# Optimization experiments

Measured on AMD Instinct MI355X. Metric: run time of the kernel, lower is better.

The kernel has to match this reference:

```python
import jax, jax.numpy as jnp
import numpy as np

H = 16       # num query heads
KV = 4       # num kv heads
D = 64       # head_dim
EPS = 1e-6


def setup_inputs() -> dict:
    key = jax.random.key(0)
    ks = jax.random.split(key, 12)
    B, N, E = 2, 2048, 1024
    s = 0.02
    return {
        "x": jax.random.normal(ks[0], (B, N, E), jnp.float32),
        "sin": jax.random.normal(ks[1], (N, D), jnp.float32),
        "cos": jax.random.normal(ks[2], (N, D), jnp.float32),
        "wq_w": jax.random.normal(ks[3], (E, E), jnp.float32) * s,
        "wq_b": jax.random.normal(ks[4], (E,), jnp.float32) * s,
        "wk_w": jax.random.normal(ks[5], (KV * D, E), jnp.float32) * s,
        "wk_b": jax.random.normal(ks[6], (KV * D,), jnp.float32) * s,
        "wv_w": jax.random.normal(ks[7], (KV * D, E), jnp.float32) * s,
        "wv_b": jax.random.normal(ks[8], (KV * D,), jnp.float32) * s,
        "qn_w": jnp.ones((D,), jnp.float32),
        "kn_w": jnp.ones((D,), jnp.float32),
        "proj_w": jax.random.normal(ks[9], (E, E), jnp.float32) * s,
        "proj_b": jax.random.normal(ks[10], (E,), jnp.float32) * s,
    }


def _rmsnorm(t, w):
    # t: [..., D]
    var = jnp.mean(t * t, axis=-1, keepdims=True)
    return t * jax.lax.rsqrt(var + EPS) * w


def _rope(t, sin, cos):
    # t: [B,h,N,D]; sin/cos: [N,D] broadcast
    x1, x2 = jnp.split(t, 2, axis=-1)
    rotated = jnp.concatenate([-x2, x1], axis=-1)
    return t * cos + rotated * sin


def reference(x, sin, cos, wq_w, wq_b, wk_w, wk_b, wv_w, wv_b,
              qn_w, kn_w, proj_w, proj_b):
    B, N, E = x.shape
    q = (x @ wq_w.T + wq_b).reshape(B, N, H, D).transpose(0, 2, 1, 3)   # [B,H,N,D]
    k = (x @ wk_w.T + wk_b).reshape(B, N, KV, D).transpose(0, 2, 1, 3)  # [B,KV,N,D]
    v = (x @ wv_w.T + wv_b).reshape(B, N, KV, D).transpose(0, 2, 1, 3)
    q = _rmsnorm(q, qn_w)
    k = _rmsnorm(k, kn_w)
    # GQA: repeat kv heads to match query heads (repeat_interleave on head dim)
    factor = H // KV
    k = jnp.repeat(k, factor, axis=1)  # [B,H,N,D]
    v = jnp.repeat(v, factor, axis=1)
    # RoPE (n_extra = 0 since sin covers full sequence)
    q = _rope(q, sin, cos)
    k = _rope(k, sin, cos)
    # scaled dot-product attention
    scale = 1.0 / np.sqrt(D).astype(np.float32)
    scores = jnp.einsum("bhqd,bhkd->bhqk", q, k) * scale
    attn = jax.nn.softmax(scores, axis=-1)
    out = jnp.einsum("bhqk,bhkd->bhqd", attn, v)      # [B,H,N,D]
    out = out.transpose(0, 2, 1, 3).reshape(B, N, E)  # [B,N,E]
    return out @ proj_w.T + proj_b
```

## Files before the change

kernel.cpp:

```cpp
#include <hip/hip_runtime.h>
#include <hip/hip_bf16.h>
#include <math.h>


#define N_SEQ 2048
#define EMB   1024
#define NH    16
#define NKV   4
#define HD    64
#define BATCH 2
#define M_TOT 4096
#define QKV_N 1536

typedef __attribute__((ext_vector_type(8)))  short short8;
typedef __attribute__((ext_vector_type(4)))  float f32x4;
typedef __attribute__((ext_vector_type(16))) float f32x16;

__device__ __forceinline__ ushort f2bf(float f) {
    union { __hip_bfloat16 h; ushort u; } cv;
    cv.h = __float2bfloat16(f);
    return cv.u;
}
__device__ __forceinline__ float bf2f(ushort u) {
    union { __hip_bfloat16 h; ushort u; } cv;
    cv.u = u;
    return __bfloat162float(cv.h);
}
__device__ __forceinline__ uint pack2bf(float a, float b) {
    union { __hip_bfloat162 h; uint u; } cv;
    cv.h = __float22bfloat162_rn(float2{a, b});
    return cv.u;
}

__device__ __forceinline__ void cvt4(const float* __restrict__ s,
                                     ushort* __restrict__ d, long g, long gd) {
    const float4 v = ((const float4*)s)[g];
    ushort4 o;
    o.x = f2bf(v.x); o.y = f2bf(v.y); o.z = f2bf(v.z); o.w = f2bf(v.w);
    ((ushort4*)d)[gd] = o;
}

__global__ __launch_bounds__(256) void prep_kernel(
    const float* __restrict__ x,  const float* __restrict__ wq,
    const float* __restrict__ wk, const float* __restrict__ wv,
    const float* __restrict__ wp, const float* __restrict__ bq,
    const float* __restrict__ bk, const float* __restrict__ bv,
    ushort* __restrict__ xb, ushort* __restrict__ Wqkv,
    ushort* __restrict__ Wproj, float* __restrict__ bqkv)
{
    const long i = (long)blockIdx.x * 256 + threadIdx.x;
    if (i < 1048576) {
        cvt4(x, xb, i, i);
    } else if (i < 1310720) {
        const long g = i - 1048576;
        cvt4(wq, Wqkv, g, g);
    } else if (i < 1376256) {
        const long g = i - 1310720;
        cvt4(wk, Wqkv, g, 262144 + g);
    } else if (i < 1441792) {
        const long g = i - 1376256;
        cvt4(wv, Wqkv, g, 327680 + g);
    } else if (i < 1703936) {
        const long g = i - 1441792;
        cvt4(wp, Wproj, g, g);
    } else if (i < 1704320) {
        const long j = i - 1703936;
        float4 v;
        if (j < 256)      v = ((const float4*)bq)[j];
        else if (j < 320) v = ((const float4*)bk)[j - 256];
        else              v = ((const float4*)bv)[j - 320];
        ((float4*)bqkv)[j] = v;
    }
}

template <bool BF16OUT>
__global__ __launch_bounds__(256) void gemm_mfma_kernel(
    const ushort* __restrict__ A, const ushort* __restrict__ W,
    const float* __restrict__ bias, void* __restrict__ Cout,
    int K, int ldc)
{
    __shared__ ushort As[128 * 40];
    __shared__ ushort Bs[128 * 40];

    const int tid = threadIdx.x;
    const int m0 = blockIdx.y * 128, n0 = blockIdx.x * 128;
    const int w = tid >> 6, lane = tid & 63;
    const int quad = lane >> 4, l16 = lane & 15;
    const int wm = (w & 1) * 64, wn = (w >> 1) * 64;

    f32x4 acc[4][4] = {};

    float bb[4];
#pragma unroll
    for (int j = 0; j < 4; ++j) bb[j] = bias[n0 + wn + j * 16 + l16];

    const int r0 = tid >> 2;
    const int c0 = tid & 3;
    const ushort* Ap = A + (size_t)(m0 + r0) * K + c0 * 8;
    const ushort* Wp = W + (size_t)(n0 + r0) * K + c0 * 8;

    for (int k0 = 0; k0 < K; k0 += 32) {
        const short8 a0 = *(const short8*)(Ap + k0);
        const short8 a1 = *(const short8*)(Ap + (size_t)64 * K + k0);
        const short8 b0 = *(const short8*)(Wp + k0);
        const short8 b1 = *(const short8*)(Wp + (size_t)64 * K + k0);
        __syncthreads();
        *(short8*)&As[r0 * 40 + c0 * 8] = a0;
        *(short8*)&As[(r0 + 64) * 40 + c0 * 8] = a1;
        *(short8*)&Bs[r0 * 40 + c0 * 8] = b0;
        *(short8*)&Bs[(r0 + 64) * 40 + c0 * 8] = b1;
        __syncthreads();

        short8 aF[4], bF[4];
#pragma unroll
        for (int i = 0; i < 4; ++i)
            aF[i] = *(const short8*)&As[(wm + i * 16 + l16) * 40 + quad * 8];
#pragma unroll
        for (int j = 0; j < 4; ++j)
            bF[j] = *(const short8*)&Bs[(wn + j * 16 + l16) * 40 + quad * 8];
#pragma unroll
        for (int i = 0; i < 4; ++i)
#pragma unroll
            for (int j = 0; j < 4; ++j)
                acc[i][j] = __builtin_amdgcn_mfma_f32_16x16x32_bf16(
                    aF[i], bF[j], acc[i][j], 0, 0, 0);
    }

#pragma unroll
    for (int i = 0; i < 4; ++i) {
        const int rowb = m0 + wm + i * 16 + quad * 4;
#pragma unroll
        for (int j = 0; j < 4; ++j) {
            const int col = n0 + wn + j * 16 + l16;
#pragma unroll
            for (int r = 0; r < 4; ++r) {
                const float vv = acc[i][j][r] + bb[j];
                if (BF16OUT)
                    ((ushort*)Cout)[(size_t)(rowb + r) * ldc + col] = f2bf(vv);
                else
                    ((float*)Cout)[(size_t)(rowb + r) * ldc + col] = vv;
            }
        }
    }
}

__global__ __launch_bounds__(256) void norm_rope_kernel(
    const ushort* __restrict__ Tq, const float* __restrict__ qn_w,
    const float* __restrict__ kn_w, const float* __restrict__ sinp,
    const float* __restrict__ cosp, ushort* __restrict__ Qb,
    ushort* __restrict__ Kf)
{
    const int gw = (int)(((long)blockIdx.x * 256 + threadIdx.x) >> 6);
    const int lane = threadIdx.x & 63;

    const bool isQ = (gw < 65536);
    const int vec = isQ ? gw : gw - 65536;
    const int hshift = isQ ? 4 : 2;
    const int colBase = isQ ? 0 : EMB;
    const float* nw = isQ ? qn_w : kn_w;
    const float outScale = isQ ? 0.125f : 1.0f;

    const int m = vec >> hshift;
    const int h = vec & ((1 << hshift) - 1);
    const int n = m & (N_SEQ - 1);
    const int b = m >> 11;

    const float t = bf2f(Tq[(size_t)m * QKV_N + colBase + h * HD + lane]);
    float s = t * t;
#pragma unroll
    for (int mask = 32; mask; mask >>= 1) s += __shfl_xor(s, mask, 64);
    const float r = rsqrtf(s * (1.0f / 64.0f) + 1e-6f);

    const float tn = t * r * nw[lane];
    const float partner = __shfl_xor(tn, 32, 64);
    const float rot = (lane < 32) ? -partner : partner;
    const float val = (tn * cosp[n * HD + lane] + rot * sinp[n * HD + lane]) * outScale;

    if (isQ) {
        Qb[((size_t)((b << 4) + h) * N_SEQ + n) * HD + lane] = f2bf(val);
    } else {
        const int kt = n >> 6, rr = n & 63, ss = rr >> 5, l32k = rr & 31;
        const int c = lane >> 4, l5k = (lane >> 3) & 1, j = lane & 7;
        Kf[((size_t)(b * NKV + h) * 32 + kt) * 4096
           + (ss * 4 + c) * 512 + l32k * 16 + l5k * 8 + j] = f2bf(val);
    }
}

__global__ __launch_bounds__(256) void transpose_v_kernel(
    const ushort* __restrict__ Tq, ushort* __restrict__ Vf)
{
    __shared__ ushort L[64 * 72];
    const int kt = blockIdx.x;
    const int n0 = kt * 64;
    const int bkv = blockIdx.y;
    const int b = bkv >> 2, kv = bkv & 3;
    const int tid = threadIdx.x;

#pragma unroll
    for (int it = 0; it < 2; ++it) {
        const int j = tid + it * 256;
        const int r = j >> 3, c = j & 7;
        const short8 v = *(const short8*)&Tq[(size_t)(b * N_SEQ + n0 + r) * QKV_N
                                             + 1280 + kv * HD + c * 8];
        *(short8*)&L[r * 72 + c * 8] = v;
    }
    __syncthreads();
#pragma unroll
    for (int it = 0; it < 2; ++it) {
        const int j = tid + it * 256;
        const int d = j >> 3, c8 = j & 7;
        short8 o;
#pragma unroll
        for (int e = 0; e < 8; ++e) o[e] = (short)L[(c8 * 8 + e) * 72 + d];
        const int ss = c8 >> 2, tt = (c8 >> 1) & 1, l5v = c8 & 1;
        const int d2 = d >> 5, l32v = d & 31;
        *(short8*)&Vf[((size_t)bkv * 32 + kt) * 4096
                      + ((ss * 2 + tt) * 2 + d2) * 512 + l32v * 16 + l5v * 8] = o;
    }
}

__global__ __launch_bounds__(256, 4) void flash_mfma32_kernel(
    const ushort* __restrict__ Qb, const ushort* __restrict__ Kf,
    const ushort* __restrict__ Vf, ushort* __restrict__ Ob)
{
    __shared__ float fsm[4352];

    const int qt = blockIdx.x;
    const int bh = blockIdx.y;
    const int b = bh >> 4, h = bh & 15;
    const int kvh = h >> 2;
    const int tid = threadIdx.x;
    const int w = tid >> 6, lane = tid & 63;
    const int l32 = lane & 31, l5 = lane >> 5;
    const int qg = w & 1;
    const int kh = w >> 1;

    const ushort* Qg = Qb + ((size_t)bh * N_SEQ + qt * 64 + qg * 32) * HD;
    const size_t kvbase = (size_t)(b * NKV + kvh) * (32 * 4096);
    const ushort* Kp = Kf + kvbase;
    const ushort* Vp = Vf + kvbase;
    const int loff = l32 * 16 + l5 * 8;

    short8 qF[4];
#pragma unroll
    for (int c = 0; c < 4; ++c)
        qF[c] = *(const short8*)&Qg[(size_t)l32 * HD + c * 16 + l5 * 8];

    f32x16 Oa[2] = {};
    float mrow = -3.0e38f, lrow = 0.0f;

    for (int i = 0; i < 16; ++i) {
        const int kt = kh * 16 + i;
        const ushort* Kt = Kp + kt * 4096;
        const ushort* Vt = Vp + kt * 4096;

        short8 kT[2][4];
#pragma unroll
        for (int s = 0; s < 2; ++s)
#pragma unroll
            for (int c = 0; c < 4; ++c)
                kT[s][c] = *(const short8*)&Kt[(s * 4 + c) * 512 + loff];
        short8 vT[2][2][2];
#pragma unroll
        for (int s = 0; s < 2; ++s)
#pragma unroll
            for (int t = 0; t < 2; ++t)
#pragma unroll
                for (int d2 = 0; d2 < 2; ++d2)
                    vT[s][t][d2] = *(const short8*)&Vt[((s * 2 + t) * 2 + d2) * 512 + loff];

        f32x16 Sv[2] = {};
#pragma unroll
        for (int s = 0; s < 2; ++s)
#pragma unroll
            for (int c = 0; c < 4; ++c)
                Sv[s] = __builtin_amdgcn_mfma_f32_32x32x16_bf16(kT[s][c], qF[c], Sv[s], 0, 0, 0);

        float mx = -3.0e38f;
#pragma unroll
        for (int s = 0; s < 2; ++s)
#pragma unroll
            for (int r = 0; r < 16; ++r) mx = fmaxf(mx, Sv[s][r]);
        mx = fmaxf(mx, __shfl_xor(mx, 32, 64));
        const float mnew = fmaxf(mrow, mx);
        const float alpha = __expf(mrow - mnew);
        mrow = mnew;
        float rs = 0.0f;
#pragma unroll
        for (int s = 0; s < 2; ++s)
#pragma unroll
            for (int r = 0; r < 16; ++r) {
                Sv[s][r] = __expf(Sv[s][r] - mnew);
                rs += Sv[s][r];
            }
        rs += __shfl_xor(rs, 32, 64);
        lrow = lrow * alpha + rs;
#pragma unroll
        for (int t = 0; t < 2; ++t)
#pragma unroll
            for (int r = 0; r < 16; ++r) Oa[t][r] *= alpha;

        uint P2[2][8];
#pragma unroll
        for (int s = 0; s < 2; ++s)
#pragma unroll
            for (int g = 0; g < 4; ++g)
#pragma unroll
                for (int hh = 0; hh < 2; ++hh)
                    P2[s][g * 2 + hh] =
                        pack2bf(Sv[s][4 * g + 2 * hh], Sv[s][4 * g + 2 * hh + 1]);

#pragma unroll
        for (int s = 0; s < 2; ++s)
#pragma unroll
            for (int t = 0; t < 2; ++t) {
                const uint snd0 = l5 ? P2[s][4 * t + 0] : P2[s][4 * t + 2];
                const uint snd1 = l5 ? P2[s][4 * t + 1] : P2[s][4 * t + 3];
                const uint kp0  = l5 ? P2[s][4 * t + 2] : P2[s][4 * t + 0];
                const uint kp1  = l5 ? P2[s][4 * t + 3] : P2[s][4 * t + 1];
                const uint rcv0 = __shfl_xor(snd0, 32, 64);
                const uint rcv1 = __shfl_xor(snd1, 32, 64);
                union { uint u[4]; short8 s8; } pb;
                pb.u[0] = l5 ? rcv0 : kp0;
                pb.u[1] = l5 ? rcv1 : kp1;
                pb.u[2] = l5 ? kp0 : rcv0;
                pb.u[3] = l5 ? kp1 : rcv1;
#pragma unroll
                for (int d2 = 0; d2 < 2; ++d2)
                    Oa[d2] = __builtin_amdgcn_mfma_f32_32x32x16_bf16(
                        vT[s][t][d2], pb.s8, Oa[d2], 0, 0, 0);
            }
    }

    float* buf = fsm + qg * 2176;
    if (kh == 1) {
#pragma unroll
        for (int d2 = 0; d2 < 2; ++d2)
#pragma unroll
            for (int r = 0; r < 16; ++r)
                buf[(d2 * 16 + r) * 64 + lane] = Oa[d2][r];
        buf[2048 + lane] = mrow;
        buf[2112 + lane] = lrow;
    }
    __syncthreads();

    if (kh == 0) {
        const float mb = buf[2048 + lane];
        const float lb = buf[2112 + lane];
        const float M = fmaxf(mrow, mb);
        const float ea = __expf(mrow - M), eb = __expf(mb - M);
        lrow = lrow * ea + lb * eb;
#pragma unroll
        for (int d2 = 0; d2 < 2; ++d2)
#pragma unroll
            for (int r = 0; r < 16; ++r)
                Oa[d2][r] = Oa[d2][r] * ea + buf[(d2 * 16 + r) * 64 + lane] * eb;
    }
    __syncthreads();

    ushort* Os = (ushort*)fsm;
    if (kh == 0) {
        const float inv = 1.0f / lrow;
#pragma unroll
        for (int d2 = 0; d2 < 2; ++d2)
#pragma unroll
            for (int r = 0; r < 16; ++r) {
                const int d = d2 * 32 + (r & 3) + 8 * (r >> 2) + 4 * l5;
                Os[(qg * 32 + l32) * 68 + d] = f2bf(Oa[d2][r] * inv);
            }
    }
    __syncthreads();

    const int row = tid >> 2, cc = (tid & 3) * 16;
#pragma unroll
    for (int i = 0; i < 2; ++i) {
        const short8 v = *(const short8*)&Os[row * 68 + cc + i * 8];
        *(short8*)&Ob[((size_t)b * N_SEQ + qt * 64 + row) * EMB + h * HD + cc + i * 8] = v;
    }
}

extern "C" void kernel_launch(void* const* d_in, const int* in_sizes, int n_in,
                              void* d_out, int out_size, void* d_ws, size_t ws_size,
                              hipStream_t stream)
{
    const float* x      = (const float*)d_in[0];
    const float* sinp   = (const float*)d_in[1];
    const float* cosp   = (const float*)d_in[2];
    const float* wq_w   = (const float*)d_in[3];
    const float* wq_b   = (const float*)d_in[4];
    const float* wk_w   = (const float*)d_in[5];
    const float* wk_b   = (const float*)d_in[6];
    const float* wv_w   = (const float*)d_in[7];
    const float* wv_b   = (const float*)d_in[8];
    const float* qn_w   = (const float*)d_in[9];
    const float* kn_w   = (const float*)d_in[10];
    const float* proj_w = (const float*)d_in[11];
    const float* proj_b = (const float*)d_in[12];
    float* out = (float*)d_out;

    ushort* Tq    = (ushort*)d_ws;
    ushort* xb    = Tq + 6291456;
    ushort* Wqkv  = xb + 4194304;
    ushort* Wproj = Wqkv + 1572864;
    float*  bqkv  = (float*)(Wproj + 1048576);
    ushort* Qb    = (ushort*)(bqkv + 1536);
    ushort* Kf    = Qb + 4194304;
    ushort* Vf    = Kf + 1048576;

    prep_kernel<<<6658, 256, 0, stream>>>(x, wq_w, wk_w, wv_w, proj_w,
                                          wq_b, wk_b, wv_b,
                                          xb, Wqkv, Wproj, bqkv);

    gemm_mfma_kernel<true><<<dim3(QKV_N / 128, M_TOT / 128), 256, 0, stream>>>(
        xb, Wqkv, bqkv, Tq, EMB, QKV_N);

    norm_rope_kernel<<<20480, 256, 0, stream>>>(Tq, qn_w, kn_w, sinp, cosp, Qb, Kf);

    transpose_v_kernel<<<dim3(32, 8), 256, 0, stream>>>(Tq, Vf);

    flash_mfma32_kernel<<<dim3(32, 32), 256, 0, stream>>>(Qb, Kf, Vf, xb);

    gemm_mfma_kernel<false><<<dim3(EMB / 128, M_TOT / 128), 256, 0, stream>>>(
        xb, Wproj, proj_b, out, EMB, EMB);
}
```

Before: 225.2 us.

## Use direct global-to-LDS loads in GEMM and split flash KV four ways

The GEMM tile loads now go straight from global memory into LDS through global_load_lds, with unpadded tiles, instead of passing through registers. The MFMA sections in the GEMM and the flash kernel are wrapped with s_setprio. The flash kernel moves to 512 threads so four waves split the KV sequence, followed by a two-level LDS merge of the partial results. The softmax folds log2e into the Q scale, uses exp2f, and skips the rescale of the running max unless the new max exceeds the old one by a threshold. The unpadded LDS tiles may cause bank conflicts, and launch bounds of (512,8) may force register spills.

```diff
diff --git a/kernel.cpp b/kernel.cpp
--- a/kernel.cpp
+++ b/kernel.cpp
@@ -30,6 +30,12 @@
     union { __hip_bfloat162 h; uint u; } cv;
     cv.h = __float22bfloat162_rn(float2{a, b});
     return cv.u;
+}
+
+__device__ __forceinline__ void g2lds16(const ushort* g, ushort* l) {
+    __builtin_amdgcn_global_load_lds(
+        (const __attribute__((address_space(1))) unsigned int*)g,
+        (__attribute__((address_space(3))) unsigned int*)l, 16, 0, 0);
 }
 
 __device__ __forceinline__ void cvt4(const float* __restrict__ s,
@@ -79,8 +85,8 @@
     const float* __restrict__ bias, void* __restrict__ Cout,
     int K, int ldc)
 {
-    __shared__ ushort As[128 * 40];
-    __shared__ ushort Bs[128 * 40];
+    __shared__ ushort As[128 * 32];
+    __shared__ ushort Bs[128 * 32];
 
     const int tid = threadIdx.x;
     const int m0 = blockIdx.y * 128, n0 = blockIdx.x * 128;
@@ -95,35 +101,35 @@
     for (int j = 0; j < 4; ++j) bb[j] = bias[n0 + wn + j * 16 + l16];
 
     const int r0 = tid >> 2;
-    const int c0 = tid & 3;
-    const ushort* Ap = A + (size_t)(m0 + r0) * K + c0 * 8;
-    const ushort* Wp = W + (size_t)(n0 + r0) * K + c0 * 8;
+    const int c8 = (tid & 3) * 8;
+    const ushort* Ap = A + (size_t)(m0 + r0) * K + c8;
+    const ushort* Wp = W + (size_t)(n0 + r0) * K + c8;
+    ushort* AsW = As + w * 512;
+    ushort* BsW = Bs + w * 512;
 
     for (int k0 = 0; k0 < K; k0 += 32) {
-        const short8 a0 = *(const short8*)(Ap + k0);
-        const short8 a1 = *(const short8*)(Ap + (size_t)64 * K + k0);
-        const short8 b0 = *(const short8*)(Wp + k0);
-        const short8 b1 = *(const short8*)(Wp + (size_t)64 * K + k0);
         __syncthreads();
-        *(short8*)&As[r0 * 40 + c0 * 8] = a0;
-        *(short8*)&As[(r0 + 64) * 40 + c0 * 8] = a1;
-        *(short8*)&Bs[r0 * 40 + c0 * 8] = b0;
-        *(short8*)&Bs[(r0 + 64) * 40 + c0 * 8] = b1;
+        g2lds16(Ap + k0, AsW);
+        g2lds16(Ap + (size_t)64 * K + k0, AsW + 2048);
+        g2lds16(Wp + k0, BsW);
+        g2lds16(Wp + (size_t)64 * K + k0, BsW + 2048);
         __syncthreads();
 
         short8 aF[4], bF[4];
 #pragma unroll
         for (int i = 0; i < 4; ++i)
-            aF[i] = *(const short8*)&As[(wm + i * 16 + l16) * 40 + quad * 8];
+            aF[i] = *(const short8*)&As[(wm + i * 16 + l16) * 32 + quad * 8];
 #pragma unroll
         for (int j = 0; j < 4; ++j)
-            bF[j] = *(const short8*)&Bs[(wn + j * 16 + l16) * 40 + quad * 8];
+            bF[j] = *(const short8*)&Bs[(wn + j * 16 + l16) * 32 + quad * 8];
+        __builtin_amdgcn_s_setprio(1);
 #pragma unroll
         for (int i = 0; i < 4; ++i)
 #pragma unroll
             for (int j = 0; j < 4; ++j)
                 acc[i][j] = __builtin_amdgcn_mfma_f32_16x16x32_bf16(
                     aF[i], bF[j], acc[i][j], 0, 0, 0);
+        __builtin_amdgcn_s_setprio(0);
     }
 
 #pragma unroll
@@ -158,7 +164,7 @@
     const int hshift = isQ ? 4 : 2;
     const int colBase = isQ ? 0 : EMB;
     const float* nw = isQ ? qn_w : kn_w;
-    const float outScale = isQ ? 0.125f : 1.0f;
+    const float outScale = isQ ? 0.125f * 1.44269504f : 1.0f;
 
     const int m = vec >> hshift;
     const int h = vec & ((1 << hshift) - 1);
@@ -219,11 +225,11 @@
     }
 }
 
-__global__ __launch_bounds__(256, 4) void flash_mfma32_kernel(
+__global__ __launch_bounds__(512, 8) void flash_mfma32_kernel(
     const ushort* __restrict__ Qb, const ushort* __restrict__ Kf,
     const ushort* __restrict__ Vf, ushort* __restrict__ Ob)
 {
-    __shared__ float fsm[4352];
+    __shared__ float fsm[8704];
 
     const int qt = blockIdx.x;
     const int bh = blockIdx.y;
@@ -249,8 +255,8 @@
     f32x16 Oa[2] = {};
     float mrow = -3.0e38f, lrow = 0.0f;
 
-    for (int i = 0; i < 16; ++i) {
-        const int kt = kh * 16 + i;
+    for (int i = 0; i < 8; ++i) {
+        const int kt = kh * 8 + i;
         const ushort* Kt = Kp + kt * 4096;
         const ushort* Vt = Vp + kt * 4096;
 
@@ -270,35 +276,42 @@
                     vT[s][t][d2] = *(const short8*)&Vt[((s * 2 + t) * 2 + d2) * 512 + loff];
 
         f32x16 Sv[2] = {};
+        __builtin_amdgcn_s_setprio(1);
 #pragma unroll
         for (int s = 0; s < 2; ++s)
 #pragma unroll
             for (int c = 0; c < 4; ++c)
                 Sv[s] = __builtin_amdgcn_mfma_f32_32x32x16_bf16(kT[s][c], qF[c], Sv[s], 0, 0, 0);
-
-        float mx = -3.0e38f;
-#pragma unroll
-        for (int s = 0; s < 2; ++s)
-#pragma unroll
-            for (int r = 0; r < 16; ++r) mx = fmaxf(mx, Sv[s][r]);
+        __builtin_amdgcn_s_setprio(0);
+
+        float mx = fmaxf(Sv[0][0], Sv[0][1]);
+#pragma unroll
+        for (int r = 2; r < 16; r += 2) mx = fmaxf(mx, fmaxf(Sv[0][r], Sv[0][r + 1]));
+#pragma unroll
+        for (int r = 0; r < 16; r += 2) mx = fmaxf(mx, fmaxf(Sv[1][r], Sv[1][r + 1]));
         mx = fmaxf(mx, __shfl_xor(mx, 32, 64));
-        const float mnew = fmaxf(mrow, mx);
-        const float alpha = __expf(mrow - mnew);
-        mrow = mnew;
+
+        if (!__all(mx <= mrow + 11.0f)) {
+            const float mnew = fmaxf(mrow, mx);
+            const float alpha = exp2f(mrow - mnew);
+            mrow = mnew;
+            lrow *= alpha;
+#pragma unroll
+            for (int t = 0; t < 2; ++t)
+#pragma unroll
+                for (int r = 0; r < 16; ++r) Oa[t][r] *= alpha;
+        }
+
         float rs = 0.0f;
 #pragma unroll
         for (int s = 0; s < 2; ++s)
 #pragma unroll
             for (int r = 0; r < 16; ++r) {
-                Sv[s][r] = __expf(Sv[s][r] - mnew);
+                Sv[s][r] = exp2f(Sv[s][r] - mrow);
                 rs += Sv[s][r];
             }
         rs += __shfl_xor(rs, 32, 64);
-        lrow = lrow * alpha + rs;
-#pragma unroll
-        for (int t = 0; t < 2; ++t)
-#pragma unroll
-            for (int r = 0; r < 16; ++r) Oa[t][r] *= alpha;
+        lrow += rs;
 
         uint P2[2][8];
 #pragma unroll
@@ -310,6 +323,7 @@
                     P2[s][g * 2 + hh] =
                         pack2bf(Sv[s][4 * g + 2 * hh], Sv[s][4 * g + 2 * hh + 1]);
 
+        __builtin_amdgcn_s_setprio(1);
 #pragma unroll
         for (int s = 0; s < 2; ++s)
 #pragma unroll
@@ -330,10 +344,10 @@
                     Oa[d2] = __builtin_amdgcn_mfma_f32_32x32x16_bf16(
                         vT[s][t][d2], pb.s8, Oa[d2], 0, 0, 0);
             }
-    }
-
-    float* buf = fsm + qg * 2176;
-    if (kh == 1) {
+        __builtin_amdgcn_s_setprio(0);
+    }
+
+    auto write_part = [&](float* buf) {
 #pragma unroll
         for (int d2 = 0; d2 < 2; ++d2)
 #pragma unroll
@@ -341,21 +355,33 @@
                 buf[(d2 * 16 + r) * 64 + lane] = Oa[d2][r];
         buf[2048 + lane] = mrow;
         buf[2112 + lane] = lrow;
-    }
-    __syncthreads();
-
-    if (kh == 0) {
+    };
+    auto merge_part = [&](const float* buf) {
         const float mb = buf[2048 + lane];
         const float lb = buf[2112 + lane];
         const float M = fmaxf(mrow, mb);
-        const float ea = __expf(mrow - M), eb = __expf(mb - M);
+        const float ea = exp2f(mrow - M), eb = exp2f(mb - M);
+        mrow = M;
         lrow = lrow * ea + lb * eb;
 #pragma unroll
         for (int d2 = 0; d2 < 2; ++d2)
 #pragma unroll
             for (int r = 0; r < 16; ++r)
                 Oa[d2][r] = Oa[d2][r] * ea + buf[(d2 * 16 + r) * 64 + lane] * eb;
-    }
+    };
+
+    float* B0 = fsm + qg * 2176;
+    float* B1 = fsm + 4352 + qg * 2176;
+
+    if (kh == 1) write_part(B0);
+    else if (kh == 3) write_part(B1);
+    __syncthreads();
+    if (kh == 0) merge_part(B0);
+    else if (kh == 2) merge_part(B1);
+    __syncthreads();
+    if (kh == 2) write_part(B0);
+    __syncthreads();
+    if (kh == 0) merge_part(B0);
     __syncthreads();
 
     ushort* Os = (ushort*)fsm;
@@ -371,12 +397,9 @@
     }
     __syncthreads();
 
-    const int row = tid >> 2, cc = (tid & 3) * 16;
-#pragma unroll
-    for (int i = 0; i < 2; ++i) {
-        const short8 v = *(const short8*)&Os[row * 68 + cc + i * 8];
-        *(short8*)&Ob[((size_t)b * N_SEQ + qt * 64 + row) * EMB + h * HD + cc + i * 8] = v;
-    }
+    const int row = tid >> 3, cc = (tid & 7) * 8;
+    const short8 v = *(const short8*)&Os[row * 68 + cc];
+    *(short8*)&Ob[((size_t)b * N_SEQ + qt * 64 + row) * EMB + h * HD + cc] = v;
 }
 
 extern "C" void kernel_launch(void* const* d_in, const int* in_sizes, int n_in,
@@ -418,7 +441,7 @@
 
     transpose_v_kernel<<<dim3(32, 8), 256, 0, stream>>>(Tq, Vf);
 
-    flash_mfma32_kernel<<<dim3(32, 32), 256, 0, stream>>>(Qb, Kf, Vf, xb);
+    flash_mfma32_kernel<<<dim3(32, 32), 512, 0, stream>>>(Qb, Kf, Vf, xb);
 
     gemm_mfma_kernel<false><<<dim3(EMB / 128, M_TOT / 128), 256, 0, stream>>>(
         xb, Wproj, proj_b, out, EMB, EMB);
```

After: 763.6 us. 239% more time.
